# Performance work log

Measured on AMD Instinct MI355X. Metric: run time of the kernel, lower is better.

Reference implementation:

```python
import jax, jax.numpy as jnp
import numpy as np

D_MODEL = 768
D_FF = 3072
N_HEADS = 12
HEAD_DIM = D_MODEL // N_HEADS
SUB_SCALE = 0.5
LN_EPS = 1e-5


def _layer_norm(x, g, b):
    mu = jnp.mean(x, axis=-1, keepdims=True)
    var = jnp.var(x, axis=-1, keepdims=True)
    return (x - mu) * jax.lax.rsqrt(var + LN_EPS) * g + b


def setup_inputs() -> dict:
    key = jax.random.key(0)
    ks = jax.random.split(key, 12)
    B, T = 1, 4096
    s = lambda fan_in: 1.0 / np.sqrt(fan_in)
    return {
        "x": jax.random.normal(ks[0], (B, T, D_MODEL), dtype=jnp.float32),
        "ln1_g": jnp.ones((D_MODEL,), jnp.float32),
        "ln1_b": jnp.zeros((D_MODEL,), jnp.float32),
        "ln2_g": jnp.ones((D_MODEL,), jnp.float32),
        "ln2_b": jnp.zeros((D_MODEL,), jnp.float32),
        "qkv_w": jax.random.normal(ks[1], (D_MODEL, 3 * D_MODEL), jnp.float32) * s(D_MODEL),
        "qkv_b": jnp.zeros((3 * D_MODEL,), jnp.float32),
        "out_w": jax.random.normal(ks[2], (D_MODEL, D_MODEL), jnp.float32) * s(D_MODEL),
        "out_b": jnp.zeros((D_MODEL,), jnp.float32),
        "fc1_w": jax.random.normal(ks[3], (D_MODEL, D_FF), jnp.float32) * s(D_MODEL),
        "fc1_b": jnp.zeros((D_FF,), jnp.float32),
        "fc2_w": jax.random.normal(ks[4], (D_FF, D_MODEL), jnp.float32) * s(D_FF),
        "fc2_b": jnp.zeros((D_MODEL,), jnp.float32),
    }


def reference(x, ln1_g, ln1_b, ln2_g, ln2_b, qkv_w, qkv_b, out_w, out_b,
              fc1_w, fc1_b, fc2_w, fc2_b):
    B, T, C = x.shape
    # --- attention sub-block ---
    h = _layer_norm(x, ln1_g, ln1_b) * SUB_SCALE
    qkv = h @ qkv_w + qkv_b                      # [B,T,3C]
    q, k, v = jnp.split(qkv, 3, axis=-1)
    split = lambda t: t.reshape(B, T, N_HEADS, HEAD_DIM).transpose(0, 2, 1, 3)
    q, k, v = split(q), split(k), split(v)       # [B,H,T,Hd]
    scores = jnp.einsum('bhqd,bhkd->bhqk', q, k) / jnp.sqrt(jnp.float32(HEAD_DIM))
    weights = jax.nn.softmax(scores, axis=-1)    # [B,H,T,T] (no mask, as in source)
    attn = jnp.einsum('bhqk,bhkd->bhqd', weights, v)
    attn = attn.transpose(0, 2, 1, 3).reshape(B, T, C)
    x = x + attn @ out_w + out_b
    # --- MLP sub-block ---
    h2 = _layer_norm(x, ln2_g, ln2_b) * SUB_SCALE
    h2 = jax.nn.gelu(h2 @ fc1_w + fc1_b, approximate=False)  # nn.GELU() = exact erf
    h2 = h2 @ fc2_w + fc2_b
    return x + h2
```

## Files before the change

kernel.cpp:

```cpp
#include <hip/hip_runtime.h>
#include <hip/hip_bf16.h>
#include <math.h>

#define TSEQ 4096
#define DMODEL 768
#define DFF 3072
#define NHEADS 12
#define HDIM 64

typedef __attribute__((ext_vector_type(8))) short short8;
typedef __attribute__((ext_vector_type(4))) float f32x4;
typedef unsigned short ushort;
typedef unsigned int uint;

typedef __attribute__((address_space(1))) ushort as1_ushort;
typedef __attribute__((address_space(3))) ushort as3_ushort;

__device__ __forceinline__ void gl_lds16(const ushort* g, const ushort* l) {
    __builtin_amdgcn_global_load_lds((as1_ushort*)(uintptr_t)g,
                                     (as3_ushort*)(uint)(uintptr_t)l, 16, 0, 0);
}

__device__ __forceinline__ ushort f2bf(float f) {
    union { float f; unsigned i; } c; c.f = f;
    unsigned x = c.i;
    unsigned r = x + 0x7FFFu + ((x >> 16) & 1u);
    return (ushort)(r >> 16);
}
__device__ __forceinline__ float asf(uint u) {
    union { unsigned i; float f; } c; c.i = u; return c.f;
}
__device__ __forceinline__ float gelu_fast(float v) {
    float y = v * (0.7978845608f + 0.03567740814f * v * v);
    float u = exp2f(y * -2.8853900817779268f);
    float r;
    asm("v_rcp_f32 %0, %1" : "=v"(r) : "v"(1.f + u));
    return v * r;
}

__global__ __launch_bounds__(256) void ln_half_kernel(
    const float* __restrict__ x, const float* __restrict__ g,
    const float* __restrict__ b, ushort* __restrict__ out)
{
    int row = blockIdx.x;
    const float* xr = x + (size_t)row * DMODEL;
    float v[3];
    float s = 0.f, s2 = 0.f;
    #pragma unroll
    for (int i = 0; i < 3; i++) {
        v[i] = xr[threadIdx.x + 256 * i];
        s += v[i]; s2 += v[i] * v[i];
    }
    #pragma unroll
    for (int m = 1; m < 64; m <<= 1) { s += __shfl_xor(s, m, 64); s2 += __shfl_xor(s2, m, 64); }
    __shared__ float ss[4], ss2[4];
    int wid = threadIdx.x >> 6;
    if ((threadIdx.x & 63) == 0) { ss[wid] = s; ss2[wid] = s2; }
    __syncthreads();
    s = ss[0] + ss[1] + ss[2] + ss[3];
    s2 = ss2[0] + ss2[1] + ss2[2] + ss2[3];
    float mu = s * (1.f / DMODEL);
    float var = s2 * (1.f / DMODEL) - mu * mu;
    float rs = rsqrtf(var + 1e-5f);
    #pragma unroll
    for (int i = 0; i < 3; i++) {
        int c = threadIdx.x + 256 * i;
        float h = (v[i] - mu) * rs * g[c] + b[c];
        out[(size_t)row * DMODEL + c] = f2bf(h * 0.5f);
    }
}

__global__ __launch_bounds__(256) void prep_kernel(
    const float* __restrict__ qkv_w, const float* __restrict__ out_w,
    const float* __restrict__ fc1_w, const float* __restrict__ fc2_w,
    const float* __restrict__ x, const float* __restrict__ ln1_g,
    const float* __restrict__ ln1_b,
    ushort* __restrict__ qkv_wT, ushort* __restrict__ out_wT,
    ushort* __restrict__ fc1_wT, ushort* __restrict__ fc2_wT,
    ushort* __restrict__ hb)
{
    __shared__ float tile[32][33];
    int bid = blockIdx.x;
    if (bid >= 6912) {
        int row = bid - 6912;
        const float* xr = x + (size_t)row * DMODEL;
        float v[3];
        float s = 0.f, s2 = 0.f;
        #pragma unroll
        for (int i = 0; i < 3; i++) {
            v[i] = xr[threadIdx.x + 256 * i];
            s += v[i]; s2 += v[i] * v[i];
        }
        #pragma unroll
        for (int m = 1; m < 64; m <<= 1) { s += __shfl_xor(s, m, 64); s2 += __shfl_xor(s2, m, 64); }
        float* ss = (float*)tile;
        int wid = threadIdx.x >> 6;
        if ((threadIdx.x & 63) == 0) { ss[wid] = s; ss[4 + wid] = s2; }
        __syncthreads();
        s = ss[0] + ss[1] + ss[2] + ss[3];
        s2 = ss[4] + ss[5] + ss[6] + ss[7];
        float mu = s * (1.f / DMODEL);
        float var = s2 * (1.f / DMODEL) - mu * mu;
        float rs = rsqrtf(var + 1e-5f);
        #pragma unroll
        for (int i = 0; i < 3; i++) {
            int c = threadIdx.x + 256 * i;
            float h = (v[i] - mu) * rs * ln1_g[c] + ln1_b[c];
            hb[(size_t)row * DMODEL + c] = f2bf(h * 0.5f);
        }
        return;
    }
    const float* in; ushort* out; int K, N, tile_id;
    if (bid < 1728)      { in = qkv_w; out = qkv_wT; K = 768;  N = 2304; tile_id = bid; }
    else if (bid < 2304) { in = out_w; out = out_wT; K = 768;  N = 768;  tile_id = bid - 1728; }
    else if (bid < 4608) { in = fc1_w; out = fc1_wT; K = 768;  N = 3072; tile_id = bid - 2304; }
    else                 { in = fc2_w; out = fc2_wT; K = 3072; N = 768;  tile_id = bid - 4608; }
    int nx = K >> 5;
    int k0 = (tile_id % nx) * 32, n0 = (tile_id / nx) * 32;

    int c = threadIdx.x & 31, r0 = threadIdx.x >> 5;
    #pragma unroll
    for (int i = 0; i < 4; i++) {
        int r = r0 + i * 8;
        tile[r][c] = in[(size_t)(k0 + r) * N + n0 + c];
    }
    __syncthreads();
    #pragma unroll
    for (int i = 0; i < 4; i++) {
        int r = r0 + i * 8;
        out[(size_t)(n0 + r) * K + k0 + c] = f2bf(tile[c][r]);
    }
}

template<int EPI>
__global__ __launch_bounds__(256) void gemm_kernel(
    const ushort* __restrict__ A, const ushort* __restrict__ Bt,
    const float* __restrict__ bias, const float* __restrict__ res,
    void* __restrict__ out, ushort* __restrict__ vTout, int M, int N, int K)
{
    __shared__ ushort As[2][128 * 32];
    __shared__ ushort Bs[2][128 * 32];
    int bm = blockIdx.x * 128, bn = blockIdx.y * 128;
    int tid = threadIdx.x;
    int wid = tid >> 6, lane = tid & 63;
    int wm = (wid >> 1) * 64, wn = (wid & 1) * 64;
    int lg = lane >> 4, lr = lane & 15;
    int srow = lane >> 2, scol = (lane & 3) * 8;
    f32x4 acc[4][4] = {};

    const ushort* ga0 = A  + (size_t)(bm + wid * 16 + srow) * K + scol;
    const ushort* ga1 = A  + (size_t)(bm + 64 + wid * 16 + srow) * K + scol;
    const ushort* gb0 = Bt + (size_t)(bn + wid * 16 + srow) * K + scol;
    const ushort* gb1 = Bt + (size_t)(bn + 64 + wid * 16 + srow) * K + scol;

    gl_lds16(ga0, &As[0][wid * 512]);
    gl_lds16(ga1, &As[0][2048 + wid * 512]);
    gl_lds16(gb0, &Bs[0][wid * 512]);
    gl_lds16(gb1, &Bs[0][2048 + wid * 512]);

    int nt = K >> 5;
    for (int t = 0; t < nt; t++) {
        int cur = t & 1;
        __syncthreads();
        if (t + 1 < nt) {
            int k0 = (t + 1) << 5;
            int nb = cur ^ 1;
            gl_lds16(ga0 + k0, &As[nb][wid * 512]);
            gl_lds16(ga1 + k0, &As[nb][2048 + wid * 512]);
            gl_lds16(gb0 + k0, &Bs[nb][wid * 512]);
            gl_lds16(gb1 + k0, &Bs[nb][2048 + wid * 512]);
        }
        short8 a[4], b[4];
        #pragma unroll
        for (int mi = 0; mi < 4; mi++) a[mi] = *(const short8*)&As[cur][(wm + mi * 16 + lr) * 32 + lg * 8];
        #pragma unroll
        for (int ni = 0; ni < 4; ni++) b[ni] = *(const short8*)&Bs[cur][(wn + ni * 16 + lr) * 32 + lg * 8];
        #pragma unroll
        for (int mi = 0; mi < 4; mi++)
            #pragma unroll
            for (int ni = 0; ni < 4; ni++)
                acc[mi][ni] = __builtin_amdgcn_mfma_f32_16x16x32_bf16(a[mi], b[ni], acc[mi][ni], 0, 0, 0);
    }

    const float C1 = 0.18033688011112042f;
    #pragma unroll
    for (int mi = 0; mi < 4; mi++) {
        #pragma unroll
        for (int ni = 0; ni < 4; ni++) {
            int col = bn + wn + ni * 16 + lr;
            float bv = bias[col];
            if (EPI == 3 && bn >= 1536) {
                int row0 = bm + wm + mi * 16 + lg * 4;
                uint2 pk;
                pk.x = (uint)f2bf(acc[mi][ni][0] + bv) | ((uint)f2bf(acc[mi][ni][1] + bv) << 16);
                pk.y = (uint)f2bf(acc[mi][ni][2] + bv) | ((uint)f2bf(acc[mi][ni][3] + bv) << 16);
                *(uint2*)&vTout[(size_t)(col - 1536) * TSEQ + row0] = pk;
            } else {
                #pragma unroll
                for (int r = 0; r < 4; r++) {
                    int row = bm + wm + mi * 16 + lg * 4 + r;
                    float v = acc[mi][ni][r] + bv;
                    size_t idx = (size_t)row * N + col;
                    if (EPI == 1) {
                        ((ushort*)out)[idx] = f2bf(gelu_fast(v));
                    } else if (EPI == 2) {
                        ((float*)out)[idx] = v + res[idx];
                    } else if (EPI == 3) {
                        ((ushort*)out)[idx] = f2bf(bn < 768 ? v * C1 : v);
                    } else {
                        ((ushort*)out)[idx] = f2bf(v);
                    }
                }
            }
        }
    }
}

template<int EPI>
__global__ __launch_bounds__(256) void gemm_64_kernel(
    const ushort* __restrict__ A, const ushort* __restrict__ Bt,
    const float* __restrict__ bias, const float* __restrict__ res,
    void* __restrict__ out, int M, int N, int K)
{
    __shared__ ushort As[2][64 * 64];
    __shared__ ushort Bs[2][64 * 64];
    int bm = blockIdx.x * 64, bn = blockIdx.y * 64;
    int tid = threadIdx.x;
    int wid = tid >> 6, lane = tid & 63;
    int wm = (wid >> 1) * 32, wn = (wid & 1) * 32;
    int lg = lane >> 4, lr = lane & 15;
    int srow = tid >> 3;
    int sunit = (tid & 7) ^ (srow & 7);
    f32x4 acc[2][2] = {};

    const ushort* ga0 = A  + (size_t)(bm + srow) * K + sunit * 8;
    const ushort* ga1 = A  + (size_t)(bm + 32 + srow) * K + sunit * 8;
    const ushort* gb0 = Bt + (size_t)(bn + srow) * K + sunit * 8;
    const ushort* gb1 = Bt + (size_t)(bn + 32 + srow) * K + sunit * 8;

    gl_lds16(ga0, &As[0][tid * 8]);
    gl_lds16(ga1, &As[0][2048 + tid * 8]);
    gl_lds16(gb0, &Bs[0][tid * 8]);
    gl_lds16(gb1, &Bs[0][2048 + tid * 8]);

    int nt = K >> 6;
    for (int t = 0; t < nt; t++) {
        int cur = t & 1;
        __syncthreads();
        if (t + 1 < nt) {
            int k0 = (t + 1) << 6;
            int nb = cur ^ 1;
            gl_lds16(ga0 + k0, &As[nb][tid * 8]);
            gl_lds16(ga1 + k0, &As[nb][2048 + tid * 8]);
            gl_lds16(gb0 + k0, &Bs[nb][tid * 8]);
            gl_lds16(gb1 + k0, &Bs[nb][2048 + tid * 8]);
        }
        #pragma unroll
        for (int h = 0; h < 2; h++) {
            short8 a[2], b[2];
            #pragma unroll
            for (int mi = 0; mi < 2; mi++) {
                int row = wm + mi * 16 + lr;
                a[mi] = *(const short8*)&As[cur][row * 64 + (((h * 4 + lg) ^ (row & 7)) * 8)];
            }
            #pragma unroll
            for (int ni = 0; ni < 2; ni++) {
                int row = wn + ni * 16 + lr;
                b[ni] = *(const short8*)&Bs[cur][row * 64 + (((h * 4 + lg) ^ (row & 7)) * 8)];
            }
            #pragma unroll
            for (int mi = 0; mi < 2; mi++)
                #pragma unroll
                for (int ni = 0; ni < 2; ni++)
                    acc[mi][ni] = __builtin_amdgcn_mfma_f32_16x16x32_bf16(a[mi], b[ni], acc[mi][ni], 0, 0, 0);
        }
    }

    #pragma unroll
    for (int mi = 0; mi < 2; mi++) {
        #pragma unroll
        for (int ni = 0; ni < 2; ni++) {
            int col = bn + wn + ni * 16 + lr;
            float bv = bias[col];
            #pragma unroll
            for (int r = 0; r < 4; r++) {
                int row = bm + wm + mi * 16 + lg * 4 + r;
                float v = acc[mi][ni][r] + bv;
                size_t idx = (size_t)row * N + col;
                if (EPI == 0) {
                    ((ushort*)out)[idx] = f2bf(v);
                } else if (EPI == 1) {
                    ((ushort*)out)[idx] = f2bf(gelu_fast(v));
                } else {
                    ((float*)out)[idx] = v + res[idx];
                }
            }
        }
    }
}

__global__ __launch_bounds__(512) void attn_kernel(
    const ushort* __restrict__ qkv, const ushort* __restrict__ vT,
    ushort* __restrict__ Opart, float* __restrict__ ml)
{
    int combo = blockIdx.x % 48;
    int qblk  = blockIdx.x / 48;
    int h     = combo >> 2;
    int split = combo & 3;
    __shared__ ushort smem[16384 + 256 * 40];
    ushort* Ps = smem + 16384;
    int tid = threadIdx.x, wid = tid >> 6, lane = tid & 63;
    int lg = lane >> 4, lr = lane & 15;
    int x7 = lr & 7;

    {
        int row = tid >> 1;
        int u0 = (tid & 1) * 4;
        int r7 = row & 7;
        const ushort* src = qkv + (size_t)(qblk * 256 + row) * 2304 + h * HDIM;
        #pragma unroll
        for (int i = 0; i < 4; i++) {
            int u = u0 + i;
            *(short8*)&smem[row * 64 + ((u ^ r7) * 8)] = *(const short8*)(src + (size_t)(u * 8));
        }
    }
    int q0row = (wid * 32 + lr) * 64;
    int q1row = q0row + 16 * 64;
    short8 qa0 = *(const short8*)&smem[q0row + (lg ^ x7) * 8];
    short8 qa1 = *(const short8*)&smem[q0row + ((4 + lg) ^ x7) * 8];
    short8 qb0 = *(const short8*)&smem[q1row + (lg ^ x7) * 8];
    short8 qb1 = *(const short8*)&smem[q1row + ((4 + lg) ^ x7) * 8];
    __syncthreads();

    short8 vone;
    #pragma unroll
    for (int i = 0; i < 8; i++) vone[i] = (short)0x3F80;

    int krow = tid >> 3;
    int kunit = (tid & 7) ^ (krow & 7);
    const ushort* kg = qkv + (size_t)(split * 1024 + krow) * 2304 + DMODEL + h * HDIM + kunit * 8;
    const ushort* vgp = vT + (size_t)(h * HDIM + krow) * TSEQ + split * 1024 + kunit * 8;

    gl_lds16(kg, &smem[tid * 8]);
    gl_lds16(vgp, &smem[8192 + tid * 8]);
    kg += 64 * 2304;
    vgp += 64;

    f32x4 o0[4] = {}, o1[4] = {};
    f32x4 s0sum = {}, s1sum = {};
    const int NT = 16;
    int prow0 = (wid * 32 + lr) * 40;
    int prow1 = prow0 + 16 * 40;

    for (int kt = 0; kt < NT; kt++) {
        int cur = kt & 1, nb = cur ^ 1;
        __syncthreads();
        if (kt + 1 < NT) {
            gl_lds16(kg, &smem[nb * 4096 + tid * 8]);
            gl_lds16(vgp, &smem[8192 + nb * 4096 + tid * 8]);
            kg += 64 * 2304;
            vgp += 64;
        }
        const ushort* kb = &smem[cur * 4096];
        const ushort* vb = &smem[8192 + cur * 4096];

        f32x4 st0[4] = {}, st1[4] = {};
        __builtin_amdgcn_s_setprio(1);
        #pragma unroll
        for (int ki = 0; ki < 4; ki++) {
            const ushort* kr = &kb[(ki * 16 + lr) * 64];
            short8 k0 = *(const short8*)&kr[(lg ^ x7) * 8];
            short8 k1 = *(const short8*)&kr[((4 + lg) ^ x7) * 8];
            st0[ki] = __builtin_amdgcn_mfma_f32_16x16x32_bf16(k0, qa0, st0[ki], 0, 0, 0);
            st0[ki] = __builtin_amdgcn_mfma_f32_16x16x32_bf16(k1, qa1, st0[ki], 0, 0, 0);
            st1[ki] = __builtin_amdgcn_mfma_f32_16x16x32_bf16(k0, qb0, st1[ki], 0, 0, 0);
            st1[ki] = __builtin_amdgcn_mfma_f32_16x16x32_bf16(k1, qb1, st1[ki], 0, 0, 0);
        }
        __builtin_amdgcn_s_setprio(0);

        uint2 c0[4], c1[4];
        #pragma unroll
        for (int ki = 0; ki < 4; ki++) {
            #pragma unroll
            for (int r = 0; r < 4; r++) st0[ki][r] = exp2f(st0[ki][r]);
            asm("v_cvt_pk_bf16_f32 %0, %1, %2" : "=v"(c0[ki].x) : "v"(st0[ki][0]), "v"(st0[ki][1]));
            asm("v_cvt_pk_bf16_f32 %0, %1, %2" : "=v"(c0[ki].y) : "v"(st0[ki][2]), "v"(st0[ki][3]));
        }
        #pragma unroll
        for (int ki = 0; ki < 4; ki++) {
            #pragma unroll
            for (int r = 0; r < 4; r++) st1[ki][r] = exp2f(st1[ki][r]);
            asm("v_cvt_pk_bf16_f32 %0, %1, %2" : "=v"(c1[ki].x) : "v"(st1[ki][0]), "v"(st1[ki][1]));
            asm("v_cvt_pk_bf16_f32 %0, %1, %2" : "=v"(c1[ki].y) : "v"(st1[ki][2]), "v"(st1[ki][3]));
        }

        *(uint2*)&Ps[prow0 + lg * 4]      = c0[0];
        *(uint2*)&Ps[prow0 + 16 + lg * 4] = c0[1];
        *(uint2*)&Ps[prow1 + lg * 4]      = c1[0];
        *(uint2*)&Ps[prow1 + 16 + lg * 4] = c1[1];
        {
            short8 pa00 = *(const short8*)&Ps[prow0 + lg * 8];
            short8 pa10 = *(const short8*)&Ps[prow1 + lg * 8];
            __builtin_amdgcn_s_setprio(1);
            s0sum = __builtin_amdgcn_mfma_f32_16x16x32_bf16(pa00, vone, s0sum, 0, 0, 0);
            s1sum = __builtin_amdgcn_mfma_f32_16x16x32_bf16(pa10, vone, s1sum, 0, 0, 0);
            #pragma unroll
            for (int ni = 0; ni < 4; ni++) {
                short8 b0 = *(const short8*)&vb[(ni * 16 + lr) * 64 + (lg ^ x7) * 8];
                o0[ni] = __builtin_amdgcn_mfma_f32_16x16x32_bf16(pa00, b0, o0[ni], 0, 0, 0);
                o1[ni] = __builtin_amdgcn_mfma_f32_16x16x32_bf16(pa10, b0, o1[ni], 0, 0, 0);
            }
            __builtin_amdgcn_s_setprio(0);
        }
        *(uint2*)&Ps[prow0 + lg * 4]      = c0[2];
        *(uint2*)&Ps[prow0 + 16 + lg * 4] = c0[3];
        *(uint2*)&Ps[prow1 + lg * 4]      = c1[2];
        *(uint2*)&Ps[prow1 + 16 + lg * 4] = c1[3];
        {
            short8 pa01 = *(const short8*)&Ps[prow0 + lg * 8];
            short8 pa11 = *(const short8*)&Ps[prow1 + lg * 8];
            __builtin_amdgcn_s_setprio(1);
            s0sum = __builtin_amdgcn_mfma_f32_16x16x32_bf16(pa01, vone, s0sum, 0, 0, 0);
            s1sum = __builtin_amdgcn_mfma_f32_16x16x32_bf16(pa11, vone, s1sum, 0, 0, 0);
            #pragma unroll
            for (int ni = 0; ni < 4; ni++) {
                short8 b1 = *(const short8*)&vb[(ni * 16 + lr) * 64 + ((4 + lg) ^ x7) * 8];
                o0[ni] = __builtin_amdgcn_mfma_f32_16x16x32_bf16(pa01, b1, o0[ni], 0, 0, 0);
                o1[ni] = __builtin_amdgcn_mfma_f32_16x16x32_bf16(pa11, b1, o1[ni], 0, 0, 0);
            }
            __builtin_amdgcn_s_setprio(0);
        }
    }

    if (lr == 0) {
        #pragma unroll
        for (int r = 0; r < 4; r++) {
            int q0 = qblk * 256 + wid * 32 + lg * 4 + r;
            ml[((size_t)split * NHEADS + h) * TSEQ + q0]      = s0sum[r];
            ml[((size_t)split * NHEADS + h) * TSEQ + q0 + 16] = s1sum[r];
        }
    }
    #pragma unroll
    for (int ni = 0; ni < 4; ni++)
        #pragma unroll
        for (int r = 0; r < 4; r++) {
            int q0 = qblk * 256 + wid * 32 + lg * 4 + r;
            int dcol = ni * 16 + lr;
            Opart[((size_t)split * TSEQ + q0) * DMODEL + h * HDIM + dcol]      = f2bf(o0[ni][r]);
            Opart[((size_t)split * TSEQ + q0 + 16) * DMODEL + h * HDIM + dcol] = f2bf(o1[ni][r]);
        }
}

__global__ __launch_bounds__(256) void attn_combine_kernel(
    const ushort* __restrict__ Opart, const float* __restrict__ ml,
    ushort* __restrict__ attnb)
{
    int gid = blockIdx.x * 256 + threadIdx.x;
    int q = gid / 96;
    int c = (gid - q * 96) * 8;
    int hh = c >> 6;
    float denom = 0.f;
    float a[8] = {};
    #pragma unroll
    for (int s = 0; s < 4; s++) {
        denom += ml[((size_t)s * NHEADS + hh) * TSEQ + q];
        uint4 ov = *(const uint4*)&Opart[((size_t)s * TSEQ + q) * DMODEL + c];
        uint w0 = ov.x, w1 = ov.y, w2 = ov.z, w3 = ov.w;
        a[0] += asf(w0 << 16); a[1] += asf(w0 & 0xFFFF0000u);
        a[2] += asf(w1 << 16); a[3] += asf(w1 & 0xFFFF0000u);
        a[4] += asf(w2 << 16); a[5] += asf(w2 & 0xFFFF0000u);
        a[6] += asf(w3 << 16); a[7] += asf(w3 & 0xFFFF0000u);
    }
    float rd = 1.f / denom;
    uint4 stv;
    stv.x = (uint)f2bf(a[0] * rd) | ((uint)f2bf(a[1] * rd) << 16);
    stv.y = (uint)f2bf(a[2] * rd) | ((uint)f2bf(a[3] * rd) << 16);
    stv.z = (uint)f2bf(a[4] * rd) | ((uint)f2bf(a[5] * rd) << 16);
    stv.w = (uint)f2bf(a[6] * rd) | ((uint)f2bf(a[7] * rd) << 16);
    *(uint4*)&attnb[(size_t)q * DMODEL + c] = stv;
}

extern "C" void kernel_launch(void* const* d_in, const int* in_sizes, int n_in,
                              void* d_out, int out_size, void* d_ws, size_t ws_size,
                              hipStream_t stream)
{
    const float* x      = (const float*)d_in[0];
    const float* ln1_g  = (const float*)d_in[1];
    const float* ln1_b  = (const float*)d_in[2];
    const float* ln2_g  = (const float*)d_in[3];
    const float* ln2_b  = (const float*)d_in[4];
    const float* qkv_w  = (const float*)d_in[5];
    const float* qkv_b  = (const float*)d_in[6];
    const float* out_w  = (const float*)d_in[7];
    const float* out_b  = (const float*)d_in[8];
    const float* fc1_w  = (const float*)d_in[9];
    const float* fc1_b  = (const float*)d_in[10];
    const float* fc2_w  = (const float*)d_in[11];
    const float* fc2_b  = (const float*)d_in[12];
    (void)in_sizes; (void)n_in; (void)out_size; (void)ws_size;

    char* p = (char*)d_ws;
    ushort* qkvb  = (ushort*)p;                 p += (size_t)TSEQ * DFF * 2;
    ushort* hb    = (ushort*)p;                 p += (size_t)TSEQ * DMODEL * 2;
    ushort* attnb = (ushort*)p;                 p += (size_t)TSEQ * DMODEL * 2;
    float*  x2    = (float*)p;                  p += (size_t)TSEQ * DMODEL * 4;
    ushort* qkv_wT = (ushort*)p;                p += (size_t)(3 * DMODEL) * DMODEL * 2;
    ushort* out_wT = (ushort*)p;                p += (size_t)DMODEL * DMODEL * 2;
    ushort* fc1_wT = (ushort*)p;                p += (size_t)DFF * DMODEL * 2;
    ushort* fc2_wT = (ushort*)p;                p += (size_t)DMODEL * DFF * 2;
    ushort* Opart  = (ushort*)p;                p += (size_t)4 * TSEQ * DMODEL * 2;
    float*  mlbuf  = (float*)p;                 p += (size_t)4 * NHEADS * TSEQ * 4;
    ushort* vTb    = (ushort*)p;                p += (size_t)DMODEL * TSEQ * 2;
    ushort* gb = qkvb;

    prep_kernel<<<11008, 256, 0, stream>>>(
        qkv_w, out_w, fc1_w, fc2_w, x, ln1_g, ln1_b,
        qkv_wT, out_wT, fc1_wT, fc2_wT, hb);

    gemm_kernel<3><<<dim3(TSEQ / 128, 3 * DMODEL / 128), 256, 0, stream>>>(
        hb, qkv_wT, qkv_b, nullptr, qkvb, vTb, TSEQ, 3 * DMODEL, DMODEL);
    attn_kernel<<<dim3((TSEQ / 256) * NHEADS * 4), 512, 0, stream>>>(qkvb, vTb, Opart, mlbuf);
    attn_combine_kernel<<<(TSEQ * DMODEL / 8) / 256, 256, 0, stream>>>(Opart, mlbuf, attnb);
    gemm_64_kernel<2><<<dim3(TSEQ / 64, DMODEL / 64), 256, 0, stream>>>(
        attnb, out_wT, out_b, x, x2, TSEQ, DMODEL, DMODEL);
    ln_half_kernel<<<TSEQ, 256, 0, stream>>>(x2, ln2_g, ln2_b, hb);
    gemm_kernel<1><<<dim3(TSEQ / 128, DFF / 128), 256, 0, stream>>>(
        hb, fc1_wT, fc1_b, nullptr, gb, nullptr, TSEQ, DFF, DMODEL);
    gemm_64_kernel<2><<<dim3(TSEQ / 64, DMODEL / 64), 256, 0, stream>>>(
        gb, fc2_wT, fc2_b, x2, (float*)d_out, TSEQ, DMODEL, DFF);
}
```

Baseline: 194.9 us.

## Restructure 128x128 GEMM to 512 threads, BK=64, XOR-swizzled LDS

The 128x128 GEMM used by the QKV and FC1 projections now runs 8 waves instead of 4, each owning a 32x64 sub-tile. The K step per stage doubles from 32 to 64, which halves the number of barriers, and the LDS layout uses an XOR swizzle on 16-byte units to avoid bank conflicts on fragment reads. The intent is more latency hiding per block and less LDS conflict overhead. In exchange, LDS use doubles to 64KB per block, which may limit how many blocks fit on a CU, and each wave has fewer accumulators to reuse each loaded fragment.

```diff
diff --git a/kernel.cpp b/kernel.cpp
--- a/kernel.cpp
+++ b/kernel.cpp
@@ -133,58 +133,68 @@
 }
 
 template<int EPI>
-__global__ __launch_bounds__(256) void gemm_kernel(
+__global__ __launch_bounds__(512) void gemm_kernel(
     const ushort* __restrict__ A, const ushort* __restrict__ Bt,
     const float* __restrict__ bias, const float* __restrict__ res,
     void* __restrict__ out, ushort* __restrict__ vTout, int M, int N, int K)
 {
-    __shared__ ushort As[2][128 * 32];
-    __shared__ ushort Bs[2][128 * 32];
+    __shared__ ushort As[2][128 * 64];
+    __shared__ ushort Bs[2][128 * 64];
     int bm = blockIdx.x * 128, bn = blockIdx.y * 128;
     int tid = threadIdx.x;
     int wid = tid >> 6, lane = tid & 63;
-    int wm = (wid >> 1) * 64, wn = (wid & 1) * 64;
+    int wm = (wid >> 1) * 32, wn = (wid & 1) * 64;
     int lg = lane >> 4, lr = lane & 15;
-    int srow = lane >> 2, scol = (lane & 3) * 8;
-    f32x4 acc[4][4] = {};
-
-    const ushort* ga0 = A  + (size_t)(bm + wid * 16 + srow) * K + scol;
-    const ushort* ga1 = A  + (size_t)(bm + 64 + wid * 16 + srow) * K + scol;
-    const ushort* gb0 = Bt + (size_t)(bn + wid * 16 + srow) * K + scol;
-    const ushort* gb1 = Bt + (size_t)(bn + 64 + wid * 16 + srow) * K + scol;
-
-    gl_lds16(ga0, &As[0][wid * 512]);
-    gl_lds16(ga1, &As[0][2048 + wid * 512]);
-    gl_lds16(gb0, &Bs[0][wid * 512]);
-    gl_lds16(gb1, &Bs[0][2048 + wid * 512]);
-
-    int nt = K >> 5;
+    int srow = tid >> 3;
+    int sunit = (tid & 7) ^ (srow & 7);
+    f32x4 acc[2][4] = {};
+
+    const ushort* ga0 = A  + (size_t)(bm + srow) * K + sunit * 8;
+    const ushort* ga1 = A  + (size_t)(bm + 64 + srow) * K + sunit * 8;
+    const ushort* gb0 = Bt + (size_t)(bn + srow) * K + sunit * 8;
+    const ushort* gb1 = Bt + (size_t)(bn + 64 + srow) * K + sunit * 8;
+
+    gl_lds16(ga0, &As[0][tid * 8]);
+    gl_lds16(ga1, &As[0][4096 + tid * 8]);
+    gl_lds16(gb0, &Bs[0][tid * 8]);
+    gl_lds16(gb1, &Bs[0][4096 + tid * 8]);
+
+    int nt = K >> 6;
     for (int t = 0; t < nt; t++) {
         int cur = t & 1;
         __syncthreads();
         if (t + 1 < nt) {
-            int k0 = (t + 1) << 5;
+            int k0 = (t + 1) << 6;
             int nb = cur ^ 1;
-            gl_lds16(ga0 + k0, &As[nb][wid * 512]);
-            gl_lds16(ga1 + k0, &As[nb][2048 + wid * 512]);
-            gl_lds16(gb0 + k0, &Bs[nb][wid * 512]);
-            gl_lds16(gb1 + k0, &Bs[nb][2048 + wid * 512]);
-        }
-        short8 a[4], b[4];
-        #pragma unroll
-        for (int mi = 0; mi < 4; mi++) a[mi] = *(const short8*)&As[cur][(wm + mi * 16 + lr) * 32 + lg * 8];
-        #pragma unroll
-        for (int ni = 0; ni < 4; ni++) b[ni] = *(const short8*)&Bs[cur][(wn + ni * 16 + lr) * 32 + lg * 8];
-        #pragma unroll
-        for (int mi = 0; mi < 4; mi++)
-            #pragma unroll
-            for (int ni = 0; ni < 4; ni++)
-                acc[mi][ni] = __builtin_amdgcn_mfma_f32_16x16x32_bf16(a[mi], b[ni], acc[mi][ni], 0, 0, 0);
+            gl_lds16(ga0 + k0, &As[nb][tid * 8]);
+            gl_lds16(ga1 + k0, &As[nb][4096 + tid * 8]);
+            gl_lds16(gb0 + k0, &Bs[nb][tid * 8]);
+            gl_lds16(gb1 + k0, &Bs[nb][4096 + tid * 8]);
+        }
+        #pragma unroll
+        for (int h = 0; h < 2; h++) {
+            short8 a[2], b[4];
+            #pragma unroll
+            for (int mi = 0; mi < 2; mi++) {
+                int row = wm + mi * 16 + lr;
+                a[mi] = *(const short8*)&As[cur][row * 64 + (((h * 4 + lg) ^ (row & 7)) * 8)];
+            }
+            #pragma unroll
+            for (int ni = 0; ni < 4; ni++) {
+                int row = wn + ni * 16 + lr;
+                b[ni] = *(const short8*)&Bs[cur][row * 64 + (((h * 4 + lg) ^ (row & 7)) * 8)];
+            }
+            #pragma unroll
+            for (int mi = 0; mi < 2; mi++)
+                #pragma unroll
+                for (int ni = 0; ni < 4; ni++)
+                    acc[mi][ni] = __builtin_amdgcn_mfma_f32_16x16x32_bf16(a[mi], b[ni], acc[mi][ni], 0, 0, 0);
+        }
     }
 
     const float C1 = 0.18033688011112042f;
     #pragma unroll
-    for (int mi = 0; mi < 4; mi++) {
+    for (int mi = 0; mi < 2; mi++) {
         #pragma unroll
         for (int ni = 0; ni < 4; ni++) {
             int col = bn + wn + ni * 16 + lr;
@@ -517,14 +527,14 @@
         qkv_w, out_w, fc1_w, fc2_w, x, ln1_g, ln1_b,
         qkv_wT, out_wT, fc1_wT, fc2_wT, hb);
 
-    gemm_kernel<3><<<dim3(TSEQ / 128, 3 * DMODEL / 128), 256, 0, stream>>>(
+    gemm_kernel<3><<<dim3(TSEQ / 128, 3 * DMODEL / 128), 512, 0, stream>>>(
         hb, qkv_wT, qkv_b, nullptr, qkvb, vTb, TSEQ, 3 * DMODEL, DMODEL);
     attn_kernel<<<dim3((TSEQ / 256) * NHEADS * 4), 512, 0, stream>>>(qkvb, vTb, Opart, mlbuf);
     attn_combine_kernel<<<(TSEQ * DMODEL / 8) / 256, 256, 0, stream>>>(Opart, mlbuf, attnb);
     gemm_64_kernel<2><<<dim3(TSEQ / 64, DMODEL / 64), 256, 0, stream>>>(
         attnb, out_wT, out_b, x, x2, TSEQ, DMODEL, DMODEL);
     ln_half_kernel<<<TSEQ, 256, 0, stream>>>(x2, ln2_g, ln2_b, hb);
-    gemm_kernel<1><<<dim3(TSEQ / 128, DFF / 128), 256, 0, stream>>>(
+    gemm_kernel<1><<<dim3(TSEQ / 128, DFF / 128), 512, 0, stream>>>(
         hb, fc1_wT, fc1_b, nullptr, gb, nullptr, TSEQ, DFF, DMODEL);
     gemm_64_kernel<2><<<dim3(TSEQ / 64, DMODEL / 64), 256, 0, stream>>>(
         gb, fc2_wT, fc2_b, x2, (float*)d_out, TSEQ, DMODEL, DFF);
```

New measurement: 203.1 us. +4.2%, slower.
